# Performance work log

Hardware: AMD Instinct MI355X
Metric: run time of the kernel (lower is better)

Reference implementation:

```python
import jax, jax.numpy as jnp
import numpy as np

B, T, D = 16, 2048, 1024
TT = T - 2            # tokens after stripping BOS/EOS
WORD_EVERY = 3        # a word starts every 3 BPE tokens
MAX_WORDS = TT // WORD_EVERY  # 682
NUM_MUTEX, NUM_BIN = 64, 32


def setup_inputs() -> dict:
    key = jax.random.key(0)
    ks = jax.random.split(key, 7)
    features = jax.random.normal(ks[0], (B, T, D), dtype=jnp.float32)
    word_starts = jnp.zeros((B, TT), dtype=jnp.int32).at[:, ::WORD_EVERY].set(1)
    s = 1.0 / np.sqrt(D)
    dense_w = jax.random.normal(ks[1], (D, D), dtype=jnp.float32) * s
    dense_b = jax.random.normal(ks[2], (D,), dtype=jnp.float32) * 0.01
    out_w = jax.random.normal(ks[3], (NUM_MUTEX, D), dtype=jnp.float32) * s
    out_b = jax.random.normal(ks[4], (NUM_MUTEX,), dtype=jnp.float32) * 0.01
    bin_w = jax.random.normal(ks[5], (NUM_BIN, D + NUM_MUTEX), dtype=jnp.float32) * s
    bin_b = jax.random.normal(ks[6], (NUM_BIN,), dtype=jnp.float32) * 0.01
    return {"features": features, "word_starts": word_starts,
            "dense_w": dense_w, "dense_b": dense_b,
            "out_w": out_w, "out_b": out_b,
            "bin_w": bin_w, "bin_b": bin_b,
            "max_words": MAX_WORDS}


def _word_features(features, word_starts, max_words):
    # strip BOS/EOS
    x = features[:, 1:-1]                                  # [B, TT, D]
    b, tt, d = x.shape
    seg = jnp.cumsum(word_starts, axis=1) - 1              # word id per token; -1 before first start
    valid = seg >= 0
    flat_seg = seg + jnp.arange(b, dtype=seg.dtype)[:, None] * max_words
    overflow = b * max_words                               # dump invalid tokens into extra bucket
    flat_seg = jnp.where(valid, flat_seg, overflow).reshape(-1)
    sums = jax.ops.segment_sum(x.reshape(-1, d), flat_seg,
                               num_segments=b * max_words + 1)[:-1]
    counts = jax.ops.segment_sum(jnp.ones((b * tt,), dtype=x.dtype), flat_seg,
                                 num_segments=b * max_words + 1)[:-1]
    sums = sums.reshape(b, max_words, d)
    counts = counts.reshape(b, max_words, 1)
    # torch code initializes word_features to ONES; empty slots stay 1.0
    return jnp.where(counts > 0, sums, jnp.ones((), dtype=x.dtype))


def reference(features, word_starts, dense_w, dense_b, out_w, out_b, bin_w, bin_b, max_words):
    wf = _word_features(features, word_starts, max_words)   # [B, MW, D]
    # dropout p=0 (eval) -> identity
    h = jnp.tanh(jnp.einsum('bwd,ed->bwe', wf, dense_w) + dense_b)
    word_class_logits = jnp.einsum('bwd,cd->bwc', h, out_w) + out_b
    cat = jnp.concatenate((word_class_logits, h), axis=-1)  # [B, MW, Cm+D]
    binary_logits = jnp.einsum('bwd,cd->bwc', cat, bin_w) + bin_b
    return (word_class_logits, binary_logits)
```

## Files before the change

kernel.cpp:

```cpp
#include <hip/hip_runtime.h>
#include <stdint.h>

#define B_   16
#define T_   2048
#define D_   1024
#define TT_  2046
#define W_   682
#define BW_  (B_ * W_)
#define NMUT 64
#define NBIN 32

typedef __attribute__((ext_vector_type(8))) short s8b;
typedef __attribute__((ext_vector_type(4))) float f32x4;

__device__ inline short f2bf(float f) {
    uint32_t u = __builtin_bit_cast(uint32_t, f);
    u += 0x7FFFu + ((u >> 16) & 1u);
    return (short)(u >> 16);
}

__device__ inline float fast_tanh(float x) {
    float xc = fminf(fmaxf(x, -15.f), 15.f);
    float e  = __expf(2.f * xc);
    return 1.f - 2.f / (e + 1.f);
}

__device__ inline void gload_lds16(const void* g, void* l) {
    __builtin_amdgcn_global_load_lds(
        (const __attribute__((address_space(1))) uint32_t*)g,
        (__attribute__((address_space(3))) uint32_t*)l, 16, 0, 0);
}

__global__ __launch_bounds__(256) void k_prep(const int* __restrict__ ws,
                                              const float* __restrict__ dw,
                                              const float* __restrict__ ow,
                                              const float* __restrict__ ob,
                                              const float* __restrict__ bw,
                                              const float* __restrict__ bb,
                                              int* __restrict__ starts,
                                              int* __restrict__ nwords,
                                              short* __restrict__ dwb,
                                              short* __restrict__ Bcat,
                                              float* __restrict__ beff) {
    __shared__ float smem[NMUT];
    int blk = blockIdx.x;
    int tid = threadIdx.x;

    if (blk < 16) {
        int b = blk;
        const int* row = ws + (size_t)b * TT_;
        int vals[8], incl[8];
        int p = 0;
        int t0 = tid * 8;
#pragma unroll
        for (int i = 0; i < 8; ++i) {
            int t = t0 + i;
            int v = (t < TT_) ? row[t] : 0;
            vals[i] = v;
            p += v;
            incl[i] = p;
        }
        int tot = p;
        int lane = tid & 63;
        int x = tot;
#pragma unroll
        for (int off = 1; off < 64; off <<= 1) {
            int v = __shfl_up(x, off);
            if (lane >= off) x += v;
        }
        int* wsum = (int*)smem;
        int wid = tid >> 6;
        if (lane == 63) wsum[wid] = x;
        __syncthreads();
        int wbase = 0;
        for (int q = 0; q < wid; ++q) wbase += wsum[q];
        int excl = wbase + x - tot;
        int* st = starts + (size_t)b * (W_ + 1);
#pragma unroll
        for (int i = 0; i < 8; ++i) {
            if (vals[i]) {
                int w = excl + incl[i] - 1;
                if (w <= W_) st[w] = t0 + i;
            }
        }
        if (tid == 0) {
            int total = wsum[0] + wsum[1] + wsum[2] + wsum[3];
            int nw = total < W_ ? total : W_;
            nwords[b] = nw;
            if (total <= W_) st[total] = TT_;
        }
    } else if (blk < 16 + 1024) {
        int i = (blk - 16) * 256 + tid;
        float4 v = ((const float4*)dw)[i];
        short4 o;
        o.x = f2bf(v.x); o.y = f2bf(v.y); o.z = f2bf(v.z); o.w = f2bf(v.w);
        *(short4*)(dwb + (size_t)i * 4) = o;
    } else if (blk < 16 + 1024 + 64) {
        int i = (blk - 1040) * 256 + tid;
        float4 v = ((const float4*)ow)[i];
        short4 o;
        o.x = f2bf(v.x); o.y = f2bf(v.y); o.z = f2bf(v.z); o.w = f2bf(v.w);
        *(short4*)(Bcat + (size_t)i * 4) = o;
    } else {
        int j = blk - 1104;
        if (tid < NMUT) smem[tid] = bw[(size_t)j * (D_ + NMUT) + tid];
        __syncthreads();
        for (int k = tid; k < D_; k += 256) {
            float acc = bw[(size_t)j * (D_ + NMUT) + NMUT + k];
#pragma unroll 8
            for (int c = 0; c < NMUT; ++c)
                acc = fmaf(smem[c], ow[(size_t)c * D_ + k], acc);
            Bcat[(size_t)(NMUT + j) * D_ + k] = f2bf(acc);
        }
        if (tid == 0) {
            float acc = bb[j];
            for (int c = 0; c < NMUT; ++c) acc = fmaf(smem[c], ob[c], acc);
            beff[j] = acc;
        }
    }
}

__global__ __launch_bounds__(256) void k_wf(const float* __restrict__ feat,
                                            const int* __restrict__ starts,
                                            const int* __restrict__ nwords,
                                            short* __restrict__ wf) {
    int blk = blockIdx.x;
    int b = blk / W_;
    int w = blk - b * W_;
    int tid = threadIdx.x;
    short* outp = wf + (size_t)blk * D_ + tid * 4;
    int nw = nwords[b];
    float4 acc = make_float4(0.f, 0.f, 0.f, 0.f);
    if (w >= nw) {
        acc = make_float4(1.f, 1.f, 1.f, 1.f);
    } else {
        const int* st = starts + (size_t)b * (W_ + 1);
        int s = st[w], e = st[w + 1];
        const float4* base = (const float4*)(feat + ((size_t)b * T_ + 1) * D_) + tid;
        for (int t = s; t < e; ++t) {
            float4 v = base[(size_t)t * (D_ / 4)];
            acc.x += v.x; acc.y += v.y; acc.z += v.z; acc.w += v.w;
        }
    }
    short4 o;
    o.x = f2bf(acc.x); o.y = f2bf(acc.y); o.z = f2bf(acc.z); o.w = f2bf(acc.w);
    *(short4*)outp = o;
}

__global__ __launch_bounds__(256) void k_gemm1(const short* __restrict__ wf,
                                               const short* __restrict__ dwb,
                                               const float* __restrict__ db,
                                               short* __restrict__ h) {
    __shared__ short As[2][128 * 32];
    __shared__ short Bs[2][128 * 32];
    int tid  = threadIdx.x;
    int lane = tid & 63;
    int w    = tid >> 6;
    int wm = w >> 1, wn = w & 1;
    int bm = blockIdx.x * 128;
    int bn = blockIdx.y * 128;

    int ln = lane & 15;
    int qk = lane >> 4;

    int srow = lane >> 2;
    int scol = (lane & 3) * 8;

    f32x4 acc[4][4];
#pragma unroll
    for (int i = 0; i < 4; ++i)
#pragma unroll
        for (int j = 0; j < 4; ++j) acc[i][j] = (f32x4){0.f, 0.f, 0.f, 0.f};

    for (int kt = 0; kt < D_; kt += 64) {
#pragma unroll
        for (int hh = 0; hh < 2; ++hh) {
#pragma unroll
            for (int p = 0; p < 2; ++p) {
                int chunk = w * 2 + p;
                int arow = bm + chunk * 16 + srow;
                arow = arow < BW_ ? arow : BW_ - 1;
                gload_lds16(wf + (size_t)arow * D_ + kt + hh * 32 + scol,
                            &As[hh][chunk * 512]);
                int brow = bn + chunk * 16 + srow;
                gload_lds16(dwb + (size_t)brow * D_ + kt + hh * 32 + scol,
                            &Bs[hh][chunk * 512]);
            }
        }
        __syncthreads();
#pragma unroll
        for (int hh = 0; hh < 2; ++hh) {
            s8b af[4], bf[4];
#pragma unroll
            for (int i = 0; i < 4; ++i)
                af[i] = *(const s8b*)&As[hh][(wm * 64 + i * 16 + ln) * 32 + qk * 8];
#pragma unroll
            for (int j = 0; j < 4; ++j)
                bf[j] = *(const s8b*)&Bs[hh][(wn * 64 + j * 16 + ln) * 32 + qk * 8];
#pragma unroll
            for (int i = 0; i < 4; ++i)
#pragma unroll
                for (int j = 0; j < 4; ++j)
                    acc[i][j] = __builtin_amdgcn_mfma_f32_16x16x32_bf16(
                        af[i], bf[j], acc[i][j], 0, 0, 0);
        }
        __syncthreads();
    }

    float bias[4];
#pragma unroll
    for (int j = 0; j < 4; ++j) bias[j] = db[bn + wn * 64 + j * 16 + ln];
#pragma unroll
    for (int i = 0; i < 4; ++i) {
        int row0 = bm + wm * 64 + i * 16 + qk * 4;
#pragma unroll
        for (int r = 0; r < 4; ++r) {
            int row = row0 + r;
            if (row < BW_) {
#pragma unroll
                for (int j = 0; j < 4; ++j) {
                    int cn = bn + wn * 64 + j * 16 + ln;
                    h[(size_t)row * D_ + cn] =
                        f2bf(fast_tanh(acc[i][j][r] + bias[j]));
                }
            }
        }
    }
}

__global__ __launch_bounds__(256) void k_gemm2(const short* __restrict__ h,
                                               const short* __restrict__ Bcat,
                                               const float* __restrict__ ob,
                                               const float* __restrict__ beff,
                                               float* __restrict__ out) {
    int tid  = threadIdx.x;
    int lane = tid & 63;
    int w    = tid >> 6;
    int ln = lane & 15, qk = lane >> 4;
    int m0 = blockIdx.x * 64 + w * 16;

    int arow = m0 + ln;
    arow = arow < BW_ ? arow : BW_ - 1;
    const short* ap = h + (size_t)arow * D_ + qk * 8;
    const short* bp = Bcat + (size_t)ln * D_ + qk * 8;

    f32x4 acc[6];
#pragma unroll
    for (int j = 0; j < 6; ++j) acc[j] = (f32x4){0.f, 0.f, 0.f, 0.f};

#pragma unroll 4
    for (int kt = 0; kt < D_; kt += 32) {
        s8b af = *(const s8b*)(ap + kt);
        s8b bf[6];
#pragma unroll
        for (int j = 0; j < 6; ++j)
            bf[j] = *(const s8b*)(bp + (size_t)j * 16 * D_ + kt);
#pragma unroll
        for (int j = 0; j < 6; ++j)
            acc[j] = __builtin_amdgcn_mfma_f32_16x16x32_bf16(af, bf[j], acc[j], 0, 0, 0);
    }

    float bj[6];
#pragma unroll
    for (int j = 0; j < 6; ++j) {
        int c = j * 16 + ln;
        bj[j] = (c < NMUT) ? ob[c] : beff[c - NMUT];
    }
#pragma unroll
    for (int r = 0; r < 4; ++r) {
        int row = m0 + qk * 4 + r;
        if (row < BW_) {
#pragma unroll
            for (int j = 0; j < 6; ++j) {
                int c = j * 16 + ln;
                float v = acc[j][r] + bj[j];
                if (c < NMUT) out[(size_t)row * NMUT + c] = v;
                else out[(size_t)BW_ * NMUT + (size_t)row * NBIN + (c - NMUT)] = v;
            }
        }
    }
}

extern "C" void kernel_launch(void* const* d_in, const int* in_sizes, int n_in,
                              void* d_out, int out_size, void* d_ws, size_t ws_size,
                              hipStream_t stream) {
    const float* feat    = (const float*)d_in[0];
    const int*   wstarts = (const int*)d_in[1];
    const float* dw      = (const float*)d_in[2];
    const float* db      = (const float*)d_in[3];
    const float* ow      = (const float*)d_in[4];
    const float* ob      = (const float*)d_in[5];
    const float* bw      = (const float*)d_in[6];
    const float* bb      = (const float*)d_in[7];
    float* out = (float*)d_out;

    char* ws = (char*)d_ws;
    size_t off = 0;
    auto alloc = [&](size_t bytes) {
        void* p = ws + off;
        off += (bytes + 255) & ~(size_t)255;
        return p;
    };
    short* wf     = (short*)alloc((size_t)BW_ * D_ * 2);
    short* h      = (short*)alloc((size_t)BW_ * D_ * 2);
    short* dwb    = (short*)alloc((size_t)D_ * D_ * 2);
    short* Bcat   = (short*)alloc((size_t)(NMUT + NBIN) * D_ * 2);
    float* beff   = (float*)alloc(NBIN * 4);
    int*   starts = (int*)alloc((size_t)B_ * (W_ + 1) * 4);
    int*   nwords = (int*)alloc(B_ * 4);

    k_prep<<<1136, 256, 0, stream>>>(wstarts, dw, ow, ob, bw, bb,
                                     starts, nwords, dwb, Bcat, beff);
    k_wf<<<BW_, 256, 0, stream>>>(feat, starts, nwords, wf);
    k_gemm1<<<dim3((BW_ + 127) / 128, D_ / 128), 256, 0, stream>>>(wf, dwb, db, h);
    k_gemm2<<<(BW_ + 63) / 64, 256, 0, stream>>>(h, Bcat, ob, beff, out);
}
```

Measured before the change: 283.2 us.

## Fuse second GEMM into first GEMM epilogue with atomic split-K accumulation

Removes the intermediate h buffer by having each GEMM1 tile stage its tanh output in LDS and immediately multiply it against the concatenated output weights. The partial results are accumulated into the zeroed output with atomicAdd across the N-tiles. Word-feature pooling, weight conversion and output zeroing are merged into one bulk kernel, with the scan split out as its own kernel, and the feature loads become nontemporal. This saves the h write and reread and one launch, but adds many float atomics and makes summation order nondeterministic.

After: 288.6 us. No clear change (+1.9%).

```diff
diff --git a/kernel.cpp b/kernel.cpp
--- a/kernel.cpp
+++ b/kernel.cpp
@@ -10,6 +10,12 @@
 #define NMUT 64
 #define NBIN 32
 
+#define G_WF   BW_
+#define G_DW   1024
+#define G_OW   64
+#define G_FOLD 32
+#define G_ZERO 1023
+
 typedef __attribute__((ext_vector_type(8))) short s8b;
 typedef __attribute__((ext_vector_type(4))) float f32x4;
 
@@ -31,78 +37,104 @@
         (__attribute__((address_space(3))) uint32_t*)l, 16, 0, 0);
 }
 
-__global__ __launch_bounds__(256) void k_prep(const int* __restrict__ ws,
+__global__ __launch_bounds__(256) void k_scan(const int* __restrict__ ws,
+                                              int* __restrict__ starts,
+                                              int* __restrict__ nwords) {
+    __shared__ int wsum[4];
+    int b = blockIdx.x;
+    int tid = threadIdx.x;
+    const int* row = ws + (size_t)b * TT_;
+    int vals[8], incl[8];
+    int p = 0;
+    int t0 = tid * 8;
+#pragma unroll
+    for (int i = 0; i < 8; ++i) {
+        int t = t0 + i;
+        int v = (t < TT_) ? row[t] : 0;
+        vals[i] = v;
+        p += v;
+        incl[i] = p;
+    }
+    int tot = p;
+    int lane = tid & 63;
+    int x = tot;
+#pragma unroll
+    for (int off = 1; off < 64; off <<= 1) {
+        int v = __shfl_up(x, off);
+        if (lane >= off) x += v;
+    }
+    int wid = tid >> 6;
+    if (lane == 63) wsum[wid] = x;
+    __syncthreads();
+    int wbase = 0;
+    for (int q = 0; q < wid; ++q) wbase += wsum[q];
+    int excl = wbase + x - tot;
+    int* st = starts + (size_t)b * (W_ + 1);
+#pragma unroll
+    for (int i = 0; i < 8; ++i) {
+        if (vals[i]) {
+            int w = excl + incl[i] - 1;
+            if (w <= W_) st[w] = t0 + i;
+        }
+    }
+    if (tid == 0) {
+        int total = wsum[0] + wsum[1] + wsum[2] + wsum[3];
+        nwords[b] = total < W_ ? total : W_;
+        if (total <= W_) st[total] = TT_;
+    }
+}
+
+__global__ __launch_bounds__(256) void k_bulk(const float* __restrict__ feat,
+                                              const int* __restrict__ starts,
+                                              const int* __restrict__ nwords,
                                               const float* __restrict__ dw,
                                               const float* __restrict__ ow,
                                               const float* __restrict__ ob,
                                               const float* __restrict__ bw,
                                               const float* __restrict__ bb,
-                                              int* __restrict__ starts,
-                                              int* __restrict__ nwords,
+                                              short* __restrict__ wf,
                                               short* __restrict__ dwb,
                                               short* __restrict__ Bcat,
-                                              float* __restrict__ beff) {
+                                              float* __restrict__ beff,
+                                              float* __restrict__ out) {
     __shared__ float smem[NMUT];
     int blk = blockIdx.x;
     int tid = threadIdx.x;
 
-    if (blk < 16) {
-        int b = blk;
-        const int* row = ws + (size_t)b * TT_;
-        int vals[8], incl[8];
-        int p = 0;
-        int t0 = tid * 8;
-#pragma unroll
-        for (int i = 0; i < 8; ++i) {
-            int t = t0 + i;
-            int v = (t < TT_) ? row[t] : 0;
-            vals[i] = v;
-            p += v;
-            incl[i] = p;
-        }
-        int tot = p;
-        int lane = tid & 63;
-        int x = tot;
-#pragma unroll
-        for (int off = 1; off < 64; off <<= 1) {
-            int v = __shfl_up(x, off);
-            if (lane >= off) x += v;
-        }
-        int* wsum = (int*)smem;
-        int wid = tid >> 6;
-        if (lane == 63) wsum[wid] = x;
-        __syncthreads();
-        int wbase = 0;
-        for (int q = 0; q < wid; ++q) wbase += wsum[q];
-        int excl = wbase + x - tot;
-        int* st = starts + (size_t)b * (W_ + 1);
-#pragma unroll
-        for (int i = 0; i < 8; ++i) {
-            if (vals[i]) {
-                int w = excl + incl[i] - 1;
-                if (w <= W_) st[w] = t0 + i;
+    if (blk < G_WF) {
+        int b = blk / W_;
+        int w = blk - b * W_;
+        short* outp = wf + (size_t)blk * D_ + tid * 4;
+        int nw = nwords[b];
+        f32x4 acc = (f32x4){0.f, 0.f, 0.f, 0.f};
+        if (w >= nw) {
+            acc = (f32x4){1.f, 1.f, 1.f, 1.f};
+        } else {
+            const int* st = starts + (size_t)b * (W_ + 1);
+            int s = st[w], e = st[w + 1];
+            const f32x4* base = (const f32x4*)(feat + ((size_t)b * T_ + 1) * D_) + tid;
+            for (int t = s; t < e; ++t) {
+                f32x4 v = __builtin_nontemporal_load(base + (size_t)t * (D_ / 4));
+                acc += v;
             }
         }
-        if (tid == 0) {
-            int total = wsum[0] + wsum[1] + wsum[2] + wsum[3];
-            int nw = total < W_ ? total : W_;
-            nwords[b] = nw;
-            if (total <= W_) st[total] = TT_;
-        }
-    } else if (blk < 16 + 1024) {
-        int i = (blk - 16) * 256 + tid;
-        float4 v = ((const float4*)dw)[i];
         short4 o;
-        o.x = f2bf(v.x); o.y = f2bf(v.y); o.z = f2bf(v.z); o.w = f2bf(v.w);
+        o.x = f2bf(acc[0]); o.y = f2bf(acc[1]); o.z = f2bf(acc[2]); o.w = f2bf(acc[3]);
+        *(short4*)outp = o;
+    } else if (blk < G_WF + G_DW) {
+        int i = (blk - G_WF) * 256 + tid;
+        f32x4 v = __builtin_nontemporal_load((const f32x4*)dw + i);
+        short4 o;
+        o.x = f2bf(v[0]); o.y = f2bf(v[1]); o.z = f2bf(v[2]); o.w = f2bf(v[3]);
         *(short4*)(dwb + (size_t)i * 4) = o;
-    } else if (blk < 16 + 1024 + 64) {
-        int i = (blk - 1040) * 256 + tid;
-        float4 v = ((const float4*)ow)[i];
+    } else if (blk < G_WF + G_DW + G_OW) {
+        int i = (blk - (G_WF + G_DW)) * 256 + tid;
+        f32x4 v = *((const f32x4*)ow + i);
         short4 o;
-        o.x = f2bf(v.x); o.y = f2bf(v.y); o.z = f2bf(v.z); o.w = f2bf(v.w);
+        o.x = f2bf(v[0]); o.y = f2bf(v[1]); o.z = f2bf(v[2]); o.w = f2bf(v[3]);
         *(short4*)(Bcat + (size_t)i * 4) = o;
-    } else {
-        int j = blk - 1104;
+    } else if (blk < G_WF + G_DW + G_OW + G_FOLD) {
+        int j = blk - (G_WF + G_DW + G_OW);
         if (tid < NMUT) smem[tid] = bw[(size_t)j * (D_ + NMUT) + tid];
         __syncthreads();
         for (int k = tid; k < D_; k += 256) {
@@ -117,42 +149,22 @@
             for (int c = 0; c < NMUT; ++c) acc = fmaf(smem[c], ob[c], acc);
             beff[j] = acc;
         }
-    }
-}
-
-__global__ __launch_bounds__(256) void k_wf(const float* __restrict__ feat,
-                                            const int* __restrict__ starts,
-                                            const int* __restrict__ nwords,
-                                            short* __restrict__ wf) {
-    int blk = blockIdx.x;
-    int b = blk / W_;
-    int w = blk - b * W_;
-    int tid = threadIdx.x;
-    short* outp = wf + (size_t)blk * D_ + tid * 4;
-    int nw = nwords[b];
-    float4 acc = make_float4(0.f, 0.f, 0.f, 0.f);
-    if (w >= nw) {
-        acc = make_float4(1.f, 1.f, 1.f, 1.f);
     } else {
-        const int* st = starts + (size_t)b * (W_ + 1);
-        int s = st[w], e = st[w + 1];
-        const float4* base = (const float4*)(feat + ((size_t)b * T_ + 1) * D_) + tid;
-        for (int t = s; t < e; ++t) {
-            float4 v = base[(size_t)t * (D_ / 4)];
-            acc.x += v.x; acc.y += v.y; acc.z += v.z; acc.w += v.w;
-        }
-    }
-    short4 o;
-    o.x = f2bf(acc.x); o.y = f2bf(acc.y); o.z = f2bf(acc.z); o.w = f2bf(acc.w);
-    *(short4*)outp = o;
+        int i = (blk - (G_WF + G_DW + G_OW + G_FOLD)) * 1024 + tid * 4;
+        *(f32x4*)(out + i) = (f32x4){0.f, 0.f, 0.f, 0.f};
+    }
 }
 
 __global__ __launch_bounds__(256) void k_gemm1(const short* __restrict__ wf,
                                                const short* __restrict__ dwb,
                                                const float* __restrict__ db,
-                                               short* __restrict__ h) {
-    __shared__ short As[2][128 * 32];
-    __shared__ short Bs[2][128 * 32];
+                                               const short* __restrict__ Bcat,
+                                               const float* __restrict__ ob,
+                                               const float* __restrict__ beff,
+                                               float* __restrict__ out) {
+    __shared__ short SMEM[16384];
+    short* As = SMEM;
+    short* Bs = SMEM + 8192;
     int tid  = threadIdx.x;
     int lane = tid & 63;
     int w    = tid >> 6;
@@ -181,10 +193,10 @@
                 int arow = bm + chunk * 16 + srow;
                 arow = arow < BW_ ? arow : BW_ - 1;
                 gload_lds16(wf + (size_t)arow * D_ + kt + hh * 32 + scol,
-                            &As[hh][chunk * 512]);
+                            &As[hh * 4096 + chunk * 512]);
                 int brow = bn + chunk * 16 + srow;
                 gload_lds16(dwb + (size_t)brow * D_ + kt + hh * 32 + scol,
-                            &Bs[hh][chunk * 512]);
+                            &Bs[hh * 4096 + chunk * 512]);
             }
         }
         __syncthreads();
@@ -193,10 +205,10 @@
             s8b af[4], bf[4];
 #pragma unroll
             for (int i = 0; i < 4; ++i)
-                af[i] = *(const s8b*)&As[hh][(wm * 64 + i * 16 + ln) * 32 + qk * 8];
+                af[i] = *(const s8b*)&As[hh * 4096 + (wm * 64 + i * 16 + ln) * 32 + qk * 8];
 #pragma unroll
             for (int j = 0; j < 4; ++j)
-                bf[j] = *(const s8b*)&Bs[hh][(wn * 64 + j * 16 + ln) * 32 + qk * 8];
+                bf[j] = *(const s8b*)&Bs[hh * 4096 + (wn * 64 + j * 16 + ln) * 32 + qk * 8];
 #pragma unroll
             for (int i = 0; i < 4; ++i)
 #pragma unroll
@@ -207,75 +219,73 @@
         __syncthreads();
     }
 
+    short* Ht = SMEM;
     float bias[4];
 #pragma unroll
     for (int j = 0; j < 4; ++j) bias[j] = db[bn + wn * 64 + j * 16 + ln];
 #pragma unroll
     for (int i = 0; i < 4; ++i) {
-        int row0 = bm + wm * 64 + i * 16 + qk * 4;
+#pragma unroll
+        for (int j = 0; j < 4; ++j) {
+            int lcol = wn * 64 + j * 16 + ln;
+#pragma unroll
+            for (int r = 0; r < 4; ++r) {
+                int lrow = wm * 64 + i * 16 + qk * 4 + r;
+                Ht[(lrow * 128 + lcol) ^ ((lrow & 7) << 3)] =
+                    f2bf(fast_tanh(acc[i][j][r] + bias[j]));
+            }
+        }
+    }
+    __syncthreads();
+
+    f32x4 accE[2][6];
+#pragma unroll
+    for (int i = 0; i < 2; ++i)
+#pragma unroll
+        for (int cj = 0; cj < 6; ++cj) accE[i][cj] = (f32x4){0.f, 0.f, 0.f, 0.f};
+
+    const short* bp = Bcat + (size_t)ln * D_ + bn + qk * 8;
+#pragma unroll
+    for (int kk = 0; kk < 4; ++kk) {
+        s8b af[2];
+#pragma unroll
+        for (int i = 0; i < 2; ++i) {
+            int row = w * 32 + i * 16 + ln;
+            int sc  = kk * 32 + qk * 8;
+            af[i] = *(const s8b*)&Ht[(row * 128 + sc) ^ ((row & 7) << 3)];
+        }
+#pragma unroll
+        for (int cj = 0; cj < 6; ++cj) {
+            s8b bf = *(const s8b*)(bp + (size_t)cj * 16 * D_ + kk * 32);
+#pragma unroll
+            for (int i = 0; i < 2; ++i)
+                accE[i][cj] = __builtin_amdgcn_mfma_f32_16x16x32_bf16(
+                    af[i], bf, accE[i][cj], 0, 0, 0);
+        }
+    }
+
+    float bj[6];
+    bool addb = (blockIdx.y == 0);
+#pragma unroll
+    for (int cj = 0; cj < 6; ++cj) {
+        int c = cj * 16 + ln;
+        bj[cj] = addb ? ((c < NMUT) ? ob[c] : beff[c - NMUT]) : 0.f;
+    }
+#pragma unroll
+    for (int i = 0; i < 2; ++i) {
 #pragma unroll
         for (int r = 0; r < 4; ++r) {
-            int row = row0 + r;
-            if (row < BW_) {
-#pragma unroll
-                for (int j = 0; j < 4; ++j) {
-                    int cn = bn + wn * 64 + j * 16 + ln;
-                    h[(size_t)row * D_ + cn] =
-                        f2bf(fast_tanh(acc[i][j][r] + bias[j]));
+            int gr = bm + w * 32 + i * 16 + qk * 4 + r;
+            if (gr < BW_) {
+#pragma unroll
+                for (int cj = 0; cj < 6; ++cj) {
+                    int c = cj * 16 + ln;
+                    float v = accE[i][cj][r] + bj[cj];
+                    if (c < NMUT)
+                        atomicAdd(&out[(size_t)gr * NMUT + c], v);
+                    else
+                        atomicAdd(&out[(size_t)BW_ * NMUT + (size_t)gr * NBIN + (c - NMUT)], v);
                 }
-            }
-        }
-    }
-}
-
-__global__ __launch_bounds__(256) void k_gemm2(const short* __restrict__ h,
-                                               const short* __restrict__ Bcat,
-                                               const float* __restrict__ ob,
-                                               const float* __restrict__ beff,
-                                               float* __restrict__ out) {
-    int tid  = threadIdx.x;
-    int lane = tid & 63;
-    int w    = tid >> 6;
-    int ln = lane & 15, qk = lane >> 4;
-    int m0 = blockIdx.x * 64 + w * 16;
-
-    int arow = m0 + ln;
-    arow = arow < BW_ ? arow : BW_ - 1;
-    const short* ap = h + (size_t)arow * D_ + qk * 8;
-    const short* bp = Bcat + (size_t)ln * D_ + qk * 8;
-
-    f32x4 acc[6];
-#pragma unroll
-    for (int j = 0; j < 6; ++j) acc[j] = (f32x4){0.f, 0.f, 0.f, 0.f};
-
-#pragma unroll 4
-    for (int kt = 0; kt < D_; kt += 32) {
-        s8b af = *(const s8b*)(ap + kt);
-        s8b bf[6];
-#pragma unroll
-        for (int j = 0; j < 6; ++j)
-            bf[j] = *(const s8b*)(bp + (size_t)j * 16 * D_ + kt);
-#pragma unroll
-        for (int j = 0; j < 6; ++j)
-            acc[j] = __builtin_amdgcn_mfma_f32_16x16x32_bf16(af, bf[j], acc[j], 0, 0, 0);
-    }
-
-    float bj[6];
-#pragma unroll
-    for (int j = 0; j < 6; ++j) {
-        int c = j * 16 + ln;
-        bj[j] = (c < NMUT) ? ob[c] : beff[c - NMUT];
-    }
-#pragma unroll
-    for (int r = 0; r < 4; ++r) {
-        int row = m0 + qk * 4 + r;
-        if (row < BW_) {
-#pragma unroll
-            for (int j = 0; j < 6; ++j) {
-                int c = j * 16 + ln;
-                float v = acc[j][r] + bj[j];
-                if (c < NMUT) out[(size_t)row * NMUT + c] = v;
-                else out[(size_t)BW_ * NMUT + (size_t)row * NBIN + (c - NMUT)] = v;
             }
         }
     }
@@ -302,16 +312,15 @@
         return p;
     };
     short* wf     = (short*)alloc((size_t)BW_ * D_ * 2);
-    short* h      = (short*)alloc((size_t)BW_ * D_ * 2);
     short* dwb    = (short*)alloc((size_t)D_ * D_ * 2);
     short* Bcat   = (short*)alloc((size_t)(NMUT + NBIN) * D_ * 2);
     float* beff   = (float*)alloc(NBIN * 4);
     int*   starts = (int*)alloc((size_t)B_ * (W_ + 1) * 4);
     int*   nwords = (int*)alloc(B_ * 4);
 
-    k_prep<<<1136, 256, 0, stream>>>(wstarts, dw, ow, ob, bw, bb,
-                                     starts, nwords, dwb, Bcat, beff);
-    k_wf<<<BW_, 256, 0, stream>>>(feat, starts, nwords, wf);
-    k_gemm1<<<dim3((BW_ + 127) / 128, D_ / 128), 256, 0, stream>>>(wf, dwb, db, h);
-    k_gemm2<<<(BW_ + 63) / 64, 256, 0, stream>>>(h, Bcat, ob, beff, out);
-}
+    k_scan<<<16, 256, 0, stream>>>(wstarts, starts, nwords);
+    k_bulk<<<G_WF + G_DW + G_OW + G_FOLD + G_ZERO, 256, 0, stream>>>(
+        feat, starts, nwords, dw, ow, ob, bw, bb, wf, dwb, Bcat, beff, out);
+    k_gemm1<<<dim3((BW_ + 127) / 128, D_ / 128), 256, 0, stream>>>(
+        wf, dwb, db, Bcat, ob, beff, out);
+}
```
